# Performance work log

Measured on AMD Instinct MI355X. Metric: run time of the kernel, lower is better.

The kernel has to match this reference:

```python
import jax, jax.numpy as jnp
import numpy as np

# SOM hyperparameters (from init_kwargs)
M_ROWS = 64
N_COLS = 64
DIM = 256
MAX_EPOCHS = 100
INITIAL_RADIUS = 32.0  # max(m, n) / 2
INITIAL_LR = 0.1
STD_COEFF = 0.5
BATCH = 8192

# [m*n, 2] integer grid locations (constant, non-differentiable)
_LOC_VECTS = jnp.asarray(
    np.stack(np.meshgrid(np.arange(M_ROWS), np.arange(N_COLS), indexing='ij'), axis=-1).reshape(-1, 2),
    dtype=jnp.int32,
)


def setup_inputs() -> dict:
    key = jax.random.key(0)
    k1, k2 = jax.random.split(key)
    return {
        'input_vect': jax.random.normal(k1, (BATCH, DIM), dtype=jnp.float32),
        'weights': jax.random.normal(k2, (M_ROWS * N_COLS, DIM), dtype=jnp.float32),
        'epoch': 10,
    }


def reference(input_vect, weights, epoch):
    # squared_distance[b, m] = sum_d (weights[m, d] - x[b, d])^2  -> [B, M]
    sq_dist = (
        jnp.sum(input_vect * input_vect, axis=1, keepdims=True)
        - 2.0 * (input_vect @ weights.T)
        + jnp.sum(weights * weights, axis=1)[None, :]
    )
    bmu_indices = jnp.argmin(sq_dist, axis=1)             # [B]
    bmu_locs = _LOC_VECTS[bmu_indices]                    # [B, 2]

    ep = jnp.float32(epoch)
    radius = INITIAL_RADIUS - ep * ((INITIAL_RADIUS - 1.0) / (MAX_EPOCHS - 1.0))
    alpha = INITIAL_LR * (1.0 - ep / MAX_EPOCHS)

    # bmu_distance_squares[b, m] = ||locs[m] - bmu_locs[b]||^2  -> [B, M]
    diff = _LOC_VECTS[None, :, :] - bmu_locs[:, None, :]  # int [B, M, 2]
    bmu_dist_sq = jnp.sum(diff * diff, axis=2).astype(jnp.float32)

    denom_nf = 2.0 * jnp.square(radius * STD_COEFF)
    learning_rate_op = jnp.exp(-bmu_dist_sq / denom_nf) * alpha  # [B, M]

    # numerator[m, d] = sum_b lr[b, m] * x[b, d]
    numerator = jnp.einsum('bm,bd->md', learning_rate_op, input_vect)
    denominator = jnp.sum(learning_rate_op, axis=0)[:, None] + 1e-12  # [M, 1]
    new_weights = numerator / denominator
    return bmu_locs, new_weights
```

## Files before the change

kernel.cpp:

```cpp
#include <hip/hip_runtime.h>
#include <stdint.h>

#define DIM   256
#define BATCH 8192
#define MCELL 4096

typedef unsigned long long u64;
typedef unsigned short u16;
typedef __attribute__((ext_vector_type(8))) short bf16x8;
typedef __attribute__((ext_vector_type(4))) float f32x4;

__device__ __forceinline__ u64 packMin(float v, unsigned idx) {
    unsigned u = __float_as_uint(v);
    u = (u & 0x80000000u) ? ~u : (u | 0x80000000u);
    return ((u64)u << 32) | (u64)idx;
}
__device__ __forceinline__ u16 f2bf(float f) {
    unsigned u = __float_as_uint(f);
    u += 0x7fffu + ((u >> 16) & 1u);
    return (u16)(u >> 16);
}
__device__ __forceinline__ void gll16(const void* g, const char* l) {
    __builtin_amdgcn_global_load_lds(
        (const __attribute__((address_space(1))) unsigned int*)g,
        (__attribute__((address_space(3))) unsigned int*)l, 16, 0, 0);
}
__device__ __forceinline__ u64 umin64(u64 a, u64 b) { return a < b ? a : b; }
__device__ __forceinline__ u64 umax64(u64 a, u64 b) { return a < b ? b : a; }
__device__ __forceinline__ void ins2(u64& t1, u64& t2, u64 p) {
    u64 hi = umax64(p, t1);
    t1 = umin64(p, t1);
    t2 = umin64(t2, hi);
}
__device__ __forceinline__ void merge2(u64& a1, u64& a2, u64 o1, u64 o2) {
    u64 H1 = umax64(a1, o1);
    a1 = umin64(a1, o1);
    a2 = umin64(H1, umin64(a2, o2));
}
__device__ __forceinline__ void merge3(u64& a1, u64& a2, u64& a3,
                                       u64 o1, u64 o2, u64 o3) {
    u64 L1 = umin64(a1, o1), H1 = umax64(a1, o1);
    u64 L2 = umin64(a2, o2);
    u64 L3 = umin64(a3, o3);
    a1 = L1;
    a2 = umin64(H1, L2);
    a3 = umin64(umax64(H1, L2), L3);
}

__global__ void k_prep(const float* __restrict__ X, const float* __restrict__ W,
                       u16* __restrict__ Xh, u16* __restrict__ Wh,
                       float* __restrict__ w2, const int* __restrict__ epoch_p,
                       float* __restrict__ scal) {
    const int blk = blockIdx.x;
    const int t = threadIdx.x;
    if (blk == 3072) {
        int raw = epoch_p[0];
        float ep = (raw >= 0 && raw < 100000) ? (float)raw : __int_as_float(raw);
        float radius = 32.0f - ep * (31.0f / 99.0f);
        float alpha  = 0.1f * (1.0f - ep / 100.0f);
        float rs = radius * 0.5f;
        float denom = 2.0f * rs * rs;
        if (t < 64)       scal[t]  = expf(-((float)(t * t)) / denom);
        else if (t == 64) scal[64] = alpha;
        return;
    }
    if (blk < 2048) {
        const int fi = blk * 256 + t;
        float4 v = ((const float4*)X)[fi];
        ushort4 h = {f2bf(v.x), f2bf(v.y), f2bf(v.z), f2bf(v.w)};
        ((ushort4*)Xh)[fi] = h;
    } else {
        const int fi = (blk - 2048) * 256 + t;
        float4 v = ((const float4*)W)[fi];
        ushort4 h = {f2bf(v.x), f2bf(v.y), f2bf(v.z), f2bf(v.w)};
        ((ushort4*)Wh)[fi] = h;
        float s = v.x * v.x + v.y * v.y + v.z * v.z + v.w * v.w;
        #pragma unroll
        for (int off = 32; off; off >>= 1) s += __shfl_down(s, off);
        if ((t & 63) == 0) w2[fi >> 6] = s;
    }
}

__global__ __launch_bounds__(256, 2)
void k_gemm_argmin(const u16* __restrict__ Xh, const u16* __restrict__ Wh,
                   const float* __restrict__ w2, u64* __restrict__ slots) {
    __shared__ char smem[65536];
    const int wg = blockIdx.x;
    const int swz = (wg & 7) * 256 + (wg >> 3);
    const int bt = swz >> 5;
    const int mt = swz & 31;
    const int tid = threadIdx.x;
    const int wid = tid >> 6;
    const int lane = tid & 63;
    const int wr = wid >> 1, wc = wid & 1;
    const int b0 = bt * 128, m0 = mt * 128;
    const int rl = lane & 15, g = lane >> 4;

    const u16* wsrc = Wh + (size_t)(m0 + wr * 64 + rl) * DIM + g * 8;
    const u16* xsrc = Xh + (size_t)(b0 + wc * 64 + rl) * DIM + g * 8;
    char* wb = smem + wid * 16384;

    f32x4 acc[4][4];
    #pragma unroll
    for (int i = 0; i < 4; ++i)
        #pragma unroll
        for (int j = 0; j < 4; ++j) acc[i][j] = (f32x4){0.f, 0.f, 0.f, 0.f};

    #define STAGE(buf, c) do {                                                \
        char* B_ = wb + (buf) * 8192;                                         \
        const int co_ = (c) * 32;                                             \
        gll16(wsrc + (size_t)0 * 16 * DIM + co_, B_ + 0 * 1024);              \
        gll16(wsrc + (size_t)1 * 16 * DIM + co_, B_ + 1 * 1024);              \
        gll16(wsrc + (size_t)2 * 16 * DIM + co_, B_ + 2 * 1024);              \
        gll16(wsrc + (size_t)3 * 16 * DIM + co_, B_ + 3 * 1024);              \
        gll16(xsrc + (size_t)0 * 16 * DIM + co_, B_ + 4 * 1024);              \
        gll16(xsrc + (size_t)1 * 16 * DIM + co_, B_ + 5 * 1024);              \
        gll16(xsrc + (size_t)2 * 16 * DIM + co_, B_ + 6 * 1024);              \
        gll16(xsrc + (size_t)3 * 16 * DIM + co_, B_ + 7 * 1024);              \
    } while (0)

    STAGE(0, 0);
    #pragma unroll
    for (int c = 0; c < 8; ++c) {
        if (c < 7) {
            STAGE((c + 1) & 1, c + 1);
            asm volatile("s_waitcnt vmcnt(8)" ::: "memory");
        } else {
            asm volatile("s_waitcnt vmcnt(0)" ::: "memory");
        }
        __builtin_amdgcn_sched_barrier(0);
        const char* bufc = wb + (c & 1) * 8192 + lane * 16;
        bf16x8 wf[4];
        #pragma unroll
        for (int i = 0; i < 4; ++i)
            wf[i] = *(const bf16x8*)(bufc + i * 1024);
        __builtin_amdgcn_s_setprio(1);
        #pragma unroll
        for (int j = 0; j < 4; ++j) {
            const bf16x8 xf = *(const bf16x8*)(bufc + (4 + j) * 1024);
            #pragma unroll
            for (int i = 0; i < 4; ++i)
                acc[i][j] = __builtin_amdgcn_mfma_f32_16x16x32_bf16(wf[i], xf, acc[i][j], 0, 0, 0);
        }
        __builtin_amdgcn_s_setprio(0);
    }
    #undef STAGE

    float w2v[16];
    #pragma unroll
    for (int ii = 0; ii < 16; ++ii)
        w2v[ii] = w2[m0 + wr * 64 + (ii >> 2) * 16 + g * 4 + (ii & 3)];

    __syncthreads();
    u64* ex = (u64*)smem;

    #pragma unroll
    for (int j = 0; j < 4; ++j) {
        u64 t1 = ~0ull, t2 = ~0ull;
        #pragma unroll
        for (int i = 0; i < 4; ++i)
            #pragma unroll
            for (int q = 0; q < 4; ++q) {
                const float d = fmaf(-2.0f, acc[i][j][q], w2v[i * 4 + q]);
                ins2(t1, t2, packMin(d, (unsigned)(m0 + wr * 64 + i * 16 + g * 4 + q)));
            }
        #pragma unroll
        for (int off = 16; off <= 32; off <<= 1) {
            const u64 o1 = __shfl_xor(t1, off);
            const u64 o2 = __shfl_xor(t2, off);
            merge2(t1, t2, o1, o2);
        }
        if (lane < 16) {
            u64* e = ex + ((size_t)(wc * 64 + j * 16 + rl) * 2 + wr) * 2;
            e[0] = t1; e[1] = t2;
        }
    }
    __syncthreads();
    if (tid < 128) {
        const u64* e = ex + (size_t)tid * 4;
        u64 a1 = e[0], a2 = e[1];
        merge2(a1, a2, e[2], e[3]);
        slots[(size_t)(b0 + tid) * 64 + mt]      = a1;
        slots[(size_t)(b0 + tid) * 64 + 32 + mt] = a2;
    }
}

__global__ void k_merge(const u64* __restrict__ slots, const float* __restrict__ X,
                        const float* __restrict__ W, const float* __restrict__ w2,
                        float* __restrict__ out_locs, int* __restrict__ bmu) {
    const int wid = threadIdx.x >> 6, l = threadIdx.x & 63;
    const int row = blockIdx.x * 4 + wid;
    u64 t1 = slots[(size_t)row * 64 + l], t2 = ~0ull, t3 = ~0ull;
    #pragma unroll
    for (int off = 1; off <= 32; off <<= 1) {
        const u64 o1 = __shfl_xor(t1, off);
        const u64 o2 = __shfl_xor(t2, off);
        const u64 o3 = __shfl_xor(t3, off);
        merge3(t1, t2, t3, o1, o2, o3);
    }
    const int cand[3] = {(int)(t1 & 0xFFFFFFFFull), (int)(t2 & 0xFFFFFFFFull),
                         (int)(t3 & 0xFFFFFFFFull)};
    const float4 xv = *(const float4*)(X + (size_t)row * DIM + l * 4);
    float bd = 0.0f; int bm = -1;
    #pragma unroll
    for (int tix = 0; tix < 3; ++tix) {
        const int mc = cand[tix];
        const float4 wv = *(const float4*)(W + (size_t)mc * DIM + l * 4);
        float s = xv.x * wv.x + xv.y * wv.y + xv.z * wv.z + xv.w * wv.w;
        #pragma unroll
        for (int off = 1; off <= 32; off <<= 1) s += __shfl_xor(s, off);
        const float d = w2[mc] - 2.0f * s;
        if (bm < 0 || d < bd || (d == bd && mc < bm)) { bd = d; bm = mc; }
    }
    if (l == 0) {
        out_locs[row * 2 + 0] = (float)(bm >> 6);
        out_locs[row * 2 + 1] = (float)(bm & 63);
        bmu[row] = bm;
    }
}

__global__ void k_gather(const int* __restrict__ bmu, const float* __restrict__ X,
                         float* __restrict__ A, float* __restrict__ cnt) {
    __shared__ int n;
    __shared__ u16 lst[BATCH];
    const int m = blockIdx.x;
    const int t = threadIdx.x;
    if (t == 0) n = 0;
    __syncthreads();
    #pragma unroll
    for (int i = 0; i < BATCH / 256; ++i) {
        const int r = i * 256 + t;
        if (bmu[r] == m) lst[atomicAdd(&n, 1)] = (u16)r;
    }
    __syncthreads();
    const int nn = n;
    float acc = 0.0f;
    for (int k = 0; k < nn; ++k)
        acc += X[(size_t)lst[k] * DIM + t];
    A[(size_t)m * DIM + t] = acc;
    if (t == 0) cnt[m] = (float)nn;
}

template<int MJQ>
__device__ __forceinline__ void conv1_body(int gi, int t, const float* __restrict__ A,
                                           const float* __restrict__ scal,
                                           float* __restrict__ T1) {
    float a[64];
    #pragma unroll
    for (int gj = 0; gj < 64; ++gj)
        a[gj] = A[(size_t)(gi * 64 + gj) * DIM + t];
    float acc[16];
    #pragma unroll
    for (int i = 0; i < 16; ++i) acc[i] = 0.0f;
    #pragma unroll
    for (int gj = 0; gj < 64; ++gj) {
        #pragma unroll
        for (int mjl = 0; mjl < 16; ++mjl) {
            const int mj = MJQ * 16 + mjl;
            const int dd = (mj >= gj) ? (mj - gj) : (gj - mj);
            acc[mjl] = fmaf(scal[dd], a[gj], acc[mjl]);
        }
    }
    #pragma unroll
    for (int mjl = 0; mjl < 16; ++mjl)
        T1[(size_t)(gi * 64 + MJQ * 16 + mjl) * DIM + t] = acc[mjl];
}

__global__ void k_conv1(const float* __restrict__ A, const float* __restrict__ scal,
                        float* __restrict__ T1, const float* __restrict__ cnt,
                        float* __restrict__ c1) {
    const int t = threadIdx.x;
    if (blockIdx.x == 64) {
        #pragma unroll
        for (int k = 0; k < 4; ++k) {
            const int o = blockIdx.y * 1024 + k * 256 + t;
            const int gi = o >> 6, mj = o & 63;
            float acc = 0.0f;
            #pragma unroll
            for (int gj = 0; gj < 64; ++gj) {
                int dd = mj - gj; dd = dd < 0 ? -dd : dd;
                acc += scal[dd] * cnt[gi * 64 + gj];
            }
            c1[o] = acc;
        }
        return;
    }
    const int gi = blockIdx.x;
    switch (blockIdx.y) {
        case 0: conv1_body<0>(gi, t, A, scal, T1); break;
        case 1: conv1_body<1>(gi, t, A, scal, T1); break;
        case 2: conv1_body<2>(gi, t, A, scal, T1); break;
        default: conv1_body<3>(gi, t, A, scal, T1); break;
    }
}

template<int MIQ>
__device__ __forceinline__ void conv2_body(int mj, int t, const float* __restrict__ T1,
                                           const float* __restrict__ scal,
                                           const float* __restrict__ c1,
                                           float* __restrict__ outw) {
    float t1r[64];
    #pragma unroll
    for (int gi = 0; gi < 64; ++gi)
        t1r[gi] = T1[(size_t)(gi * 64 + mj) * DIM + t];
    __shared__ float dens[16];
    if (t < 16) {
        const int mi = MIQ * 16 + t;
        float dn = 0.0f;
        #pragma unroll
        for (int gi = 0; gi < 64; ++gi) {
            int dd = mi - gi; dd = dd < 0 ? -dd : dd;
            dn = fmaf(scal[dd], c1[gi * 64 + mj], dn);
        }
        dens[t] = dn;
    }
    __syncthreads();
    float acc[16];
    #pragma unroll
    for (int i = 0; i < 16; ++i) acc[i] = 0.0f;
    #pragma unroll
    for (int gi = 0; gi < 64; ++gi) {
        #pragma unroll
        for (int mil = 0; mil < 16; ++mil) {
            const int mi = MIQ * 16 + mil;
            const int dd = (mi >= gi) ? (mi - gi) : (gi - mi);
            acc[mil] = fmaf(scal[dd], t1r[gi], acc[mil]);
        }
    }
    const float al = scal[64];
    #pragma unroll
    for (int mil = 0; mil < 16; ++mil) {
        const int mi = MIQ * 16 + mil;
        outw[(size_t)(mi * 64 + mj) * DIM + t] = (al * acc[mil]) / (al * dens[mil] + 1e-12f);
    }
}

__global__ void k_conv2(const float* __restrict__ T1, const float* __restrict__ scal,
                        const float* __restrict__ c1, float* __restrict__ outw) {
    const int t = threadIdx.x;
    const int mj = blockIdx.x;
    switch (blockIdx.y) {
        case 0: conv2_body<0>(mj, t, T1, scal, c1, outw); break;
        case 1: conv2_body<1>(mj, t, T1, scal, c1, outw); break;
        case 2: conv2_body<2>(mj, t, T1, scal, c1, outw); break;
        default: conv2_body<3>(mj, t, T1, scal, c1, outw); break;
    }
}

extern "C" void kernel_launch(void* const* d_in, const int* in_sizes, int n_in,
                              void* d_out, int out_size, void* d_ws, size_t ws_size,
                              hipStream_t stream) {
    const float* X = (const float*)d_in[0];
    const float* W = (const float*)d_in[1];
    const int*   ep = (const int*)d_in[2];
    float* out = (float*)d_out;

    char* ws = (char*)d_ws;
    u64*   slots = (u64*)(ws + 0);
    float* T1    = (float*)(ws + 0);
    u16*   Xh    = (u16*)(ws + (4u << 20));
    float* A     = (float*)(ws + (4u << 20));
    float* cnt   = (float*)(ws + (8u << 20));
    u16*   Wh    = (u16*)(ws + (8u << 20) + 16384);
    float* w2    = (float*)(ws + (10u << 20) + 16384);
    float* scal  = (float*)(ws + (10u << 20) + 32768);
    float* c1    = (float*)(ws + (10u << 20) + 36864);
    int*   bmu   = (int*)(ws + (10u << 20) + 53248);

    k_prep<<<3073, 256, 0, stream>>>(X, W, Xh, Wh, w2, ep, scal);
    k_gemm_argmin<<<2048, 256, 0, stream>>>(Xh, Wh, w2, slots);
    k_merge<<<2048, 256, 0, stream>>>(slots, X, W, w2, out, bmu);
    k_gather<<<MCELL, 256, 0, stream>>>(bmu, X, A, cnt);
    k_conv1<<<dim3(65, 4), 256, 0, stream>>>(A, scal, T1, cnt, c1);
    k_conv2<<<dim3(64, 4), 256, 0, stream>>>(T1, scal, c1, out + 16384);
}
```

Measured before the change: 185.9 us.

## Restage GEMM X tile in LDS, coarsen gather, split conv register loads

The GEMM kernel now stages the whole shared 128x256 X tile into LDS up front with an XOR swizzle, so every wave reads it from LDS. The W fragments are loaded straight from global into registers with one-step prefetch, replacing the double-buffered per-wave staging of both operands. The gather kernel handles four cells per block with int4 scans of the BMU array, cutting redundant full-batch scans but adding a filtered loop over the list. Both conv kernels load their 64 inputs in two halves of 32 to lower register pressure, and conv2 moves its barrier later so the density computation overlaps the main loop.

Result: slower. 234.9 us (+26.3%).

```diff
diff --git a/kernel.cpp b/kernel.cpp
--- a/kernel.cpp
+++ b/kernel.cpp
@@ -96,9 +96,22 @@
     const int b0 = bt * 128, m0 = mt * 128;
     const int rl = lane & 15, g = lane >> 4;
 
+    const int sr0 = wid * 32 + (lane >> 2);
+    const int sr1 = sr0 + 16;
+    const int ss  = lane & 3;
+    const int sg0 = ss ^ ((sr0 >> 1) & 3);
+    const int sg1 = ss ^ ((sr1 >> 1) & 3);
+    const size_t gA0 = (size_t)(b0 + sr0) * DIM + sg0 * 8;
+    const size_t gA1 = (size_t)(b0 + sr1) * DIM + sg1 * 8;
+    const int ldsA = wid * 2048;
+    #pragma unroll
+    for (int c = 0; c < 8; ++c) {
+        char* base_ = smem + c * 8192;
+        gll16(Xh + gA0 + c * 32, base_ + ldsA);
+        gll16(Xh + gA1 + c * 32, base_ + ldsA + 1024);
+    }
+
     const u16* wsrc = Wh + (size_t)(m0 + wr * 64 + rl) * DIM + g * 8;
-    const u16* xsrc = Xh + (size_t)(b0 + wc * 64 + rl) * DIM + g * 8;
-    char* wb = smem + wid * 16384;
 
     f32x4 acc[4][4];
     #pragma unroll
@@ -106,45 +119,37 @@
         #pragma unroll
         for (int j = 0; j < 4; ++j) acc[i][j] = (f32x4){0.f, 0.f, 0.f, 0.f};
 
-    #define STAGE(buf, c) do {                                                \
-        char* B_ = wb + (buf) * 8192;                                         \
-        const int co_ = (c) * 32;                                             \
-        gll16(wsrc + (size_t)0 * 16 * DIM + co_, B_ + 0 * 1024);              \
-        gll16(wsrc + (size_t)1 * 16 * DIM + co_, B_ + 1 * 1024);              \
-        gll16(wsrc + (size_t)2 * 16 * DIM + co_, B_ + 2 * 1024);              \
-        gll16(wsrc + (size_t)3 * 16 * DIM + co_, B_ + 3 * 1024);              \
-        gll16(xsrc + (size_t)0 * 16 * DIM + co_, B_ + 4 * 1024);              \
-        gll16(xsrc + (size_t)1 * 16 * DIM + co_, B_ + 5 * 1024);              \
-        gll16(xsrc + (size_t)2 * 16 * DIM + co_, B_ + 6 * 1024);              \
-        gll16(xsrc + (size_t)3 * 16 * DIM + co_, B_ + 7 * 1024);              \
-    } while (0)
-
-    STAGE(0, 0);
+    __syncthreads();
+
+    const int slot = g ^ ((rl >> 1) & 3);
+    const int xoff = (wc * 64 + rl) * 64 + slot * 16;
+
+    bf16x8 wf[4];
+    #pragma unroll
+    for (int i = 0; i < 4; ++i)
+        wf[i] = *(const bf16x8*)(wsrc + (size_t)i * 16 * DIM);
+
     #pragma unroll
     for (int c = 0; c < 8; ++c) {
+        bf16x8 wn[4];
         if (c < 7) {
-            STAGE((c + 1) & 1, c + 1);
-            asm volatile("s_waitcnt vmcnt(8)" ::: "memory");
-        } else {
-            asm volatile("s_waitcnt vmcnt(0)" ::: "memory");
-        }
-        __builtin_amdgcn_sched_barrier(0);
-        const char* bufc = wb + (c & 1) * 8192 + lane * 16;
-        bf16x8 wf[4];
-        #pragma unroll
-        for (int i = 0; i < 4; ++i)
-            wf[i] = *(const bf16x8*)(bufc + i * 1024);
-        __builtin_amdgcn_s_setprio(1);
+            #pragma unroll
+            for (int i = 0; i < 4; ++i)
+                wn[i] = *(const bf16x8*)(wsrc + (size_t)i * 16 * DIM + (c + 1) * 32);
+        }
+        const char* bufc = smem + c * 8192;
         #pragma unroll
         for (int j = 0; j < 4; ++j) {
-            const bf16x8 xf = *(const bf16x8*)(bufc + (4 + j) * 1024);
+            const bf16x8 xf = *(const bf16x8*)(bufc + xoff + j * 1024);
             #pragma unroll
             for (int i = 0; i < 4; ++i)
                 acc[i][j] = __builtin_amdgcn_mfma_f32_16x16x32_bf16(wf[i], xf, acc[i][j], 0, 0, 0);
         }
-        __builtin_amdgcn_s_setprio(0);
-    }
-    #undef STAGE
+        if (c < 7) {
+            #pragma unroll
+            for (int i = 0; i < 4; ++i) wf[i] = wn[i];
+        }
+    }
 
     float w2v[16];
     #pragma unroll
@@ -223,42 +228,58 @@
                          float* __restrict__ A, float* __restrict__ cnt) {
     __shared__ int n;
     __shared__ u16 lst[BATCH];
-    const int m = blockIdx.x;
+    const int bx = blockIdx.x;
     const int t = threadIdx.x;
     if (t == 0) n = 0;
     __syncthreads();
-    #pragma unroll
-    for (int i = 0; i < BATCH / 256; ++i) {
-        const int r = i * 256 + t;
-        if (bmu[r] == m) lst[atomicAdd(&n, 1)] = (u16)r;
+    const int4* b4 = (const int4*)bmu;
+    #pragma unroll
+    for (int i = 0; i < BATCH / 4 / 256; ++i) {
+        const int idx = i * 256 + t;
+        const int4 v = b4[idx];
+        const int mv[4] = {v.x, v.y, v.z, v.w};
+        #pragma unroll
+        for (int q = 0; q < 4; ++q)
+            if ((mv[q] >> 2) == bx)
+                lst[atomicAdd(&n, 1)] = (u16)(((idx * 4 + q) << 2) | (mv[q] & 3));
     }
     __syncthreads();
     const int nn = n;
-    float acc = 0.0f;
-    for (int k = 0; k < nn; ++k)
-        acc += X[(size_t)lst[k] * DIM + t];
-    A[(size_t)m * DIM + t] = acc;
-    if (t == 0) cnt[m] = (float)nn;
+    #pragma unroll
+    for (int cc = 0; cc < 4; ++cc) {
+        float acc = 0.0f; int kc = 0;
+        for (int k = 0; k < nn; ++k) {
+            const u16 e = lst[k];
+            if ((e & 3) == cc) { acc += X[(size_t)(e >> 2) * DIM + t]; ++kc; }
+        }
+        const int m = bx * 4 + cc;
+        A[(size_t)m * DIM + t] = acc;
+        if (t == 0) cnt[m] = (float)kc;
+    }
 }
 
 template<int MJQ>
 __device__ __forceinline__ void conv1_body(int gi, int t, const float* __restrict__ A,
                                            const float* __restrict__ scal,
                                            float* __restrict__ T1) {
-    float a[64];
-    #pragma unroll
-    for (int gj = 0; gj < 64; ++gj)
-        a[gj] = A[(size_t)(gi * 64 + gj) * DIM + t];
     float acc[16];
     #pragma unroll
     for (int i = 0; i < 16; ++i) acc[i] = 0.0f;
     #pragma unroll
-    for (int gj = 0; gj < 64; ++gj) {
-        #pragma unroll
-        for (int mjl = 0; mjl < 16; ++mjl) {
-            const int mj = MJQ * 16 + mjl;
-            const int dd = (mj >= gj) ? (mj - gj) : (gj - mj);
-            acc[mjl] = fmaf(scal[dd], a[gj], acc[mjl]);
+    for (int h = 0; h < 2; ++h) {
+        float a[32];
+        #pragma unroll
+        for (int g2 = 0; g2 < 32; ++g2)
+            a[g2] = A[(size_t)(gi * 64 + h * 32 + g2) * DIM + t];
+        #pragma unroll
+        for (int g2 = 0; g2 < 32; ++g2) {
+            const int gj = h * 32 + g2;
+            #pragma unroll
+            for (int mjl = 0; mjl < 16; ++mjl) {
+                const int mj = MJQ * 16 + mjl;
+                const int dd = (mj >= gj) ? (mj - gj) : (gj - mj);
+                acc[mjl] = fmaf(scal[dd], a[g2], acc[mjl]);
+            }
         }
     }
     #pragma unroll
@@ -299,34 +320,37 @@
                                            const float* __restrict__ scal,
                                            const float* __restrict__ c1,
                                            float* __restrict__ outw) {
-    float t1r[64];
-    #pragma unroll
-    for (int gi = 0; gi < 64; ++gi)
-        t1r[gi] = T1[(size_t)(gi * 64 + mj) * DIM + t];
     __shared__ float dens[16];
     if (t < 16) {
         const int mi = MIQ * 16 + t;
         float dn = 0.0f;
-        #pragma unroll
         for (int gi = 0; gi < 64; ++gi) {
             int dd = mi - gi; dd = dd < 0 ? -dd : dd;
             dn = fmaf(scal[dd], c1[gi * 64 + mj], dn);
         }
         dens[t] = dn;
     }
-    __syncthreads();
     float acc[16];
     #pragma unroll
     for (int i = 0; i < 16; ++i) acc[i] = 0.0f;
     #pragma unroll
-    for (int gi = 0; gi < 64; ++gi) {
-        #pragma unroll
-        for (int mil = 0; mil < 16; ++mil) {
-            const int mi = MIQ * 16 + mil;
-            const int dd = (mi >= gi) ? (mi - gi) : (gi - mi);
-            acc[mil] = fmaf(scal[dd], t1r[gi], acc[mil]);
-        }
-    }
+    for (int h = 0; h < 2; ++h) {
+        float t1r[32];
+        #pragma unroll
+        for (int g2 = 0; g2 < 32; ++g2)
+            t1r[g2] = T1[(size_t)((h * 32 + g2) * 64 + mj) * DIM + t];
+        #pragma unroll
+        for (int g2 = 0; g2 < 32; ++g2) {
+            const int gi = h * 32 + g2;
+            #pragma unroll
+            for (int mil = 0; mil < 16; ++mil) {
+                const int mi = MIQ * 16 + mil;
+                const int dd = (mi >= gi) ? (mi - gi) : (gi - mi);
+                acc[mil] = fmaf(scal[dd], t1r[g2], acc[mil]);
+            }
+        }
+    }
+    __syncthreads();
     const float al = scal[64];
     #pragma unroll
     for (int mil = 0; mil < 16; ++mil) {
@@ -370,7 +394,7 @@
     k_prep<<<3073, 256, 0, stream>>>(X, W, Xh, Wh, w2, ep, scal);
     k_gemm_argmin<<<2048, 256, 0, stream>>>(Xh, Wh, w2, slots);
     k_merge<<<2048, 256, 0, stream>>>(slots, X, W, w2, out, bmu);
-    k_gather<<<MCELL, 256, 0, stream>>>(bmu, X, A, cnt);
+    k_gather<<<1024, 256, 0, stream>>>(bmu, X, A, cnt);
     k_conv1<<<dim3(65, 4), 256, 0, stream>>>(A, scal, T1, cnt, c1);
     k_conv2<<<dim3(64, 4), 256, 0, stream>>>(T1, scal, c1, out + 16384);
 }
```
